# Performance work log

Hardware: AMD Instinct MI355X
Metric: run time of the kernel (lower is better)

The kernel has to match this reference:

```python
import jax, jax.numpy as jnp
import numpy as np

NUM_HEADS = 8
NUM_GROUPS = 8
EPS = 1e-5


def group_norm(x, weight, bias):
    B, C, T, H, W = x.shape
    xg = x.reshape(B, NUM_GROUPS, C // NUM_GROUPS, T, H, W)
    mean = xg.mean(axis=(2, 3, 4, 5), keepdims=True)
    var = xg.var(axis=(2, 3, 4, 5), keepdims=True)
    xg = (xg - mean) * jax.lax.rsqrt(var + EPS)
    x = xg.reshape(B, C, T, H, W)
    return x * weight[None, :, None, None, None] + bias[None, :, None, None, None]


def setup_inputs() -> dict:
    key = jax.random.key(0)
    ks = jax.random.split(key, 5)
    B, C, T, H, W = 4, 512, 16, 32, 32
    x = jax.random.normal(ks[0], (B, C, T, H, W), dtype=jnp.float32)
    gn_weight = jnp.ones((C,), dtype=jnp.float32)
    gn_bias = jnp.zeros((C,), dtype=jnp.float32)
    # 1x1x1 Conv3d weights collapse to dense (out, in) matrices
    qkv_w = jax.random.normal(ks[1], (3 * C, C), dtype=jnp.float32) * (1.0 / np.sqrt(C))
    qkv_b = jax.random.normal(ks[2], (3 * C,), dtype=jnp.float32) * 0.02
    out_w = jax.random.normal(ks[3], (C, C), dtype=jnp.float32) * (1.0 / np.sqrt(C))
    out_b = jax.random.normal(ks[4], (C,), dtype=jnp.float32) * 0.02
    return {"x": x, "gn_weight": gn_weight, "gn_bias": gn_bias,
            "qkv_w": qkv_w, "qkv_b": qkv_b, "out_w": out_w, "out_b": out_b}


def reference(x, gn_weight, gn_bias, qkv_w, qkv_b, out_w, out_b):
    B, C, T, H, W = x.shape
    nh = NUM_HEADS
    d = C // nh
    N = T * H * W

    h = group_norm(x, gn_weight, gn_bias)

    # 1x1x1 conv == pointwise channel matmul
    hf = h.reshape(B, C, N)                                  # [B, C, N]
    qkv = jnp.einsum('oc,bcn->bon', qkv_w, hf) + qkv_b[None, :, None]
    q, k, v = jnp.split(qkv, 3, axis=1)                      # each [B, C, N]
    q = q.reshape(B, nh, d, N)
    k = k.reshape(B, nh, d, N)
    v = v.reshape(B, nh, d, N)

    # NOTE: faithful to the torch code — contraction is over N (tokens),
    # giving a [B, nh, d, d] channel-attention matrix; softmax over last d.
    scale = d ** (-0.5)
    attn = jnp.einsum('bhdn,bhen->bhde', q, k) * scale       # [B, nh, d, d]
    attn = jax.nn.softmax(attn, axis=-1)
    out = jnp.einsum('bhde,bhen->bhdn', attn, v)             # [B, nh, d, N]

    out = out.reshape(B, C, N)
    out = jnp.einsum('oc,bcn->bon', out_w, out) + out_b[None, :, None]
    out = out.reshape(B, C, T, H, W)
    return x + out
```

## Files before the change

### kernel.cpp

```cpp
#include <hip/hip_runtime.h>
#include <hip/hip_fp16.h>


#define CCH 512
#define NTOK 16384
#define NHEAD 8

typedef _Float16 f16;
typedef _Float16 f16x8 __attribute__((ext_vector_type(8)));
typedef float f32x4 __attribute__((ext_vector_type(4)));

__device__ __forceinline__ void g2l16(const void* g, void* l) {
  __builtin_amdgcn_global_load_lds((const __attribute__((address_space(1))) void*)g,
                                   (__attribute__((address_space(3))) void*)l,
                                   16, 0, 0);
}

__global__ __launch_bounds__(256) void k_prep(const float* __restrict__ x,
                                              float* __restrict__ stats,
                                              const float* __restrict__ qkvw,
                                              f16* __restrict__ Wqkv16,
                                              const float* __restrict__ outw,
                                              f16* __restrict__ Ow16,
                                              f16* __restrict__ Wvt16) {
  __shared__ __align__(16) char smp[9216];
  int bid = blockIdx.x;
  int t = threadIdx.x;
  if (bid < 1024) {
    int chunk = bid & 31, bg = bid >> 5;
    const float4* p = (const float4*)(x + (size_t)bg * (64ull * NTOK)) + (size_t)chunk * 8192;
    float s = 0.f, q = 0.f;
    for (int i = t; i < 8192; i += 256) {
      float4 v = p[i];
      s += v.x + v.y + v.z + v.w;
      q += v.x * v.x + v.y * v.y + v.z * v.z + v.w * v.w;
    }
    for (int off = 32; off; off >>= 1) { s += __shfl_down(s, off); q += __shfl_down(q, off); }
    float* ls = (float*)smp; float* lq = ls + 4;
    int wid = t >> 6, lane = t & 63;
    if (lane == 0) { ls[wid] = s; lq[wid] = q; }
    __syncthreads();
    if (t == 0) {
      atomicAdd(&stats[bg * 2 + 0], ls[0] + ls[1] + ls[2] + ls[3]);
      atomicAdd(&stats[bg * 2 + 1], lq[0] + lq[1] + lq[2] + lq[3]);
    }
  } else if (bid < 2048) {
    bool isB = bid >= 1792;
    int i = (isB ? (bid - 1792) : (bid - 1024)) * 256 + t;
    const float* src = isB ? outw : qkvw;
    f16* dst = isB ? Ow16 : Wqkv16;
    float4 v = *(const float4*)&src[i * 4];
    f16 h[4] __attribute__((aligned(8)));
    h[0] = (f16)v.x; h[1] = (f16)v.y; h[2] = (f16)v.z; h[3] = (f16)v.w;
    *(uint2*)&dst[i * 4] = *(const uint2*)h;
  } else {
    int j = bid - 2048;
    int et = j >> 3, ct = j & 7;
    f16 (*tl)[72] = (f16(*)[72])smp;
    int r = t >> 2, cq = (t & 3) * 16;
    const float* src = &qkvw[(size_t)(1024 + et * 64 + r) * CCH + ct * 64 + cq];
#pragma unroll
    for (int k = 0; k < 4; ++k) {
      float4 v = *(const float4*)(src + k * 4);
      tl[r][cq + k * 4 + 0] = (f16)v.x; tl[r][cq + k * 4 + 1] = (f16)v.y;
      tl[r][cq + k * 4 + 2] = (f16)v.z; tl[r][cq + k * 4 + 3] = (f16)v.w;
    }
    __syncthreads();
    f16 hv[16] __attribute__((aligned(16)));
#pragma unroll
    for (int jj = 0; jj < 16; ++jj) hv[jj] = tl[cq + jj][r];
    f16* dst = &Wvt16[(size_t)(ct * 64 + r) * CCH + et * 64 + cq];
    *(uint4*)&dst[0] = ((const uint4*)hv)[0];
    *(uint4*)&dst[8] = ((const uint4*)hv)[1];
  }
}

__global__ __launch_bounds__(256) void k_gnorm(const float* __restrict__ x,
                                               const float* __restrict__ gw,
                                               const float* __restrict__ gb,
                                               const float* __restrict__ stats,
                                               f16* __restrict__ H, f16* __restrict__ Ht,
                                               float* __restrict__ svec) {
  int nc = blockIdx.x;
  int cg = blockIdx.y;
  int b = blockIdx.z;
  int t = threadIdx.x;
  __shared__ f16 T2[64][260];
  __shared__ float svp[4][64];
  float sum = stats[(b * 8 + cg) * 2], sq = stats[(b * 8 + cg) * 2 + 1];
  const float inv = 1.f / (64.f * (float)NTOK);
  float mean = sum * inv;
  float var = fmaxf(sq * inv - mean * mean, 0.f);
  float rsig = rsqrtf(var + 1e-5f);
  int c0 = cg * 64, n0 = nc * 256;
  int tq = t & 63, rr0 = t >> 6;
#pragma unroll
  for (int it = 0; it < 16; ++it) {
    int r = it * 4 + rr0;
    int c = c0 + r;
    float a = gw[c] * rsig;
    float bb = gb[c] - mean * a;
    size_t idx = ((size_t)(b * CCH + c)) * NTOK + n0 + tq * 4;
    float4 xv = *(const float4*)&x[idx];
    f16 hh[4] __attribute__((aligned(8)));
    hh[0] = (f16)(xv.x * a + bb);
    hh[1] = (f16)(xv.y * a + bb);
    hh[2] = (f16)(xv.z * a + bb);
    hh[3] = (f16)(xv.w * a + bb);
    *(uint2*)&H[idx] = *(const uint2*)hh;
    *(uint2*)&T2[r][tq * 4] = *(const uint2*)hh;
  }
  __syncthreads();
  {
    int c = t & 63, q = t >> 6;
    float acc = 0.f;
#pragma unroll
    for (int j = 0; j < 64; ++j) acc += (float)T2[c][q * 64 + j];
    svp[q][c] = acc;
  }
  __syncthreads();
  if (t < 64) {
    atomicAdd(&svec[b * CCH + c0 + t],
              svp[0][t] + svp[1][t] + svp[2][t] + svp[3][t]);
  }
  int s8 = t & 7, nl = t >> 3;
#pragma unroll
  for (int it = 0; it < 8; ++it) {
    int n = it * 32 + nl;
    f16 g[8] __attribute__((aligned(16)));
#pragma unroll
    for (int j = 0; j < 8; ++j) g[j] = T2[s8 * 8 + j][n];
    *(uint4*)&Ht[((size_t)b * NTOK + n0 + n) * CCH + c0 + s8 * 8] = *(const uint4*)g;
  }
}

#define SPLITS 16
__global__ __launch_bounds__(256, 2) void k_syrk(const f16* __restrict__ H,
                                                 float* __restrict__ G) {
  const int TI[10] = {0, 0, 0, 0, 1, 1, 1, 2, 2, 3};
  const int TJ[10] = {0, 1, 2, 3, 1, 2, 3, 2, 3, 3};
  int tile = blockIdx.x;
  int split = blockIdx.y;
  int b = blockIdx.z;
  int ii = TI[tile], jj = TJ[tile];
  int m0 = ii * 128, n0 = jj * 128;
  int t = threadIdx.x, lane = t & 63, wid = t >> 6;
  int wr = wid >> 1, wc = wid & 1;
  __shared__ __align__(16) f16 sA[128 * 64];
  __shared__ __align__(16) f16 sB[128 * 64];
  const f16* Hb = H + (size_t)b * CCH * NTOK;
  int k0 = split * (NTOK / SPLITS);
  f32x4 acc[4][4] = {};
  int ldsrow = wid * 8 + (lane >> 3);
  int slot = lane & 7;
  int lr = lane & 15, lk = lane >> 4;

  const int NS = (NTOK / SPLITS) / 64;
  for (int ks = 0; ks < NS; ++ks) {
    int kk0 = k0 + ks * 64;
    __syncthreads();
#pragma unroll
    for (int i = 0; i < 4; ++i) {
      int row = ldsrow + i * 32;
      int cA = ((slot ^ (row & 7)) * 8);
      g2l16(Hb + (size_t)(m0 + row) * NTOK + kk0 + cA, &sA[i * 2048 + wid * 512]);
      g2l16(Hb + (size_t)(n0 + row) * NTOK + kk0 + cA, &sB[i * 2048 + wid * 512]);
    }
    asm volatile("s_waitcnt vmcnt(0)" ::: "memory");
    __syncthreads();
#pragma unroll
    for (int kk = 0; kk < 2; ++kk) {
      f16x8 af[4], bf[4];
#pragma unroll
      for (int mi = 0; mi < 4; ++mi) {
        int row = wr * 64 + mi * 16 + lr;
        int ks8 = (kk * 4 + lk) ^ (row & 7);
        af[mi] = *(const f16x8*)&sA[row * 64 + ks8 * 8];
      }
#pragma unroll
      for (int ni = 0; ni < 4; ++ni) {
        int row = wc * 64 + ni * 16 + lr;
        int ks8 = (kk * 4 + lk) ^ (row & 7);
        bf[ni] = *(const f16x8*)&sB[row * 64 + ks8 * 8];
      }
#pragma unroll
      for (int mi = 0; mi < 4; ++mi)
#pragma unroll
        for (int ni = 0; ni < 4; ++ni)
          acc[mi][ni] = __builtin_amdgcn_mfma_f32_16x16x32_f16(af[mi], bf[ni], acc[mi][ni], 0, 0, 0);
    }
  }

  float* Gb = G + (size_t)b * CCH * CCH;
#pragma unroll
  for (int mi = 0; mi < 4; ++mi)
#pragma unroll
    for (int j = 0; j < 4; ++j) {
      int rr2 = m0 + wr * 64 + mi * 16 + lk * 4 + j;
#pragma unroll
      for (int ni = 0; ni < 4; ++ni) {
        int cc = n0 + wc * 64 + ni * 16 + lr;
        atomicAdd(&Gb[(size_t)rr2 * CCH + cc], acc[mi][ni][j]);
      }
    }
}

__global__ __launch_bounds__(256) void k_symm(float* __restrict__ G,
                                              f16* __restrict__ G16) {
  const int TI6[6] = {0, 0, 0, 1, 1, 2};
  const int TJ6[6] = {1, 2, 3, 2, 3, 3};
  int bx = blockIdx.x;
  int b = blockIdx.y;
  float* Gb = G + (size_t)b * CCH * CCH;
  f16* Gh = G16 + (size_t)b * CCH * CCH;
  __shared__ float s[64][65];
  int t = threadIdx.x;
  int r = t >> 2, cg = (t & 3) * 16;
  int ib, jb;
  bool mirror = bx < 24;
  if (mirror) {
    int t6 = bx >> 2, sub = bx & 3;
    ib = TI6[t6] * 2 + (sub >> 1); jb = TJ6[t6] * 2 + (sub & 1);
  } else {
    int idx = bx - 24; int dt = idx >> 2, sub = idx & 3;
    ib = dt * 2 + (sub >> 1); jb = dt * 2 + (sub & 1);
  }
  int grow = ib * 64 + r, gcol0 = jb * 64 + cg;
  const float* src = &Gb[(size_t)grow * CCH + gcol0];
  f16 hv[16] __attribute__((aligned(16)));
#pragma unroll
  for (int k = 0; k < 4; ++k) {
    float4 v = *(const float4*)(src + k * 4);
    if (mirror) {
      s[r][cg + k * 4 + 0] = v.x; s[r][cg + k * 4 + 1] = v.y;
      s[r][cg + k * 4 + 2] = v.z; s[r][cg + k * 4 + 3] = v.w;
    }
    hv[k * 4 + 0] = (f16)(v.x - ((grow == gcol0 + k * 4 + 0) ? 16384.f : 0.f));
    hv[k * 4 + 1] = (f16)(v.y - ((grow == gcol0 + k * 4 + 1) ? 16384.f : 0.f));
    hv[k * 4 + 2] = (f16)(v.z - ((grow == gcol0 + k * 4 + 2) ? 16384.f : 0.f));
    hv[k * 4 + 3] = (f16)(v.w - ((grow == gcol0 + k * 4 + 3) ? 16384.f : 0.f));
  }
  f16* d16 = &Gh[(size_t)grow * CCH + gcol0];
  *(uint4*)&d16[0] = ((const uint4*)hv)[0];
  *(uint4*)&d16[8] = ((const uint4*)hv)[1];
  if (mirror) {
    __syncthreads();
    float* dst = &Gb[(size_t)(jb * 64 + r) * CCH + ib * 64 + cg];
    f16 hw[16] __attribute__((aligned(16)));
#pragma unroll
    for (int k = 0; k < 4; ++k) {
      float4 v;
      v.x = s[cg + k * 4 + 0][r]; v.y = s[cg + k * 4 + 1][r];
      v.z = s[cg + k * 4 + 2][r]; v.w = s[cg + k * 4 + 3][r];
      *(float4*)(dst + k * 4) = v;
      hw[k * 4 + 0] = (f16)v.x; hw[k * 4 + 1] = (f16)v.y;
      hw[k * 4 + 2] = (f16)v.z; hw[k * 4 + 3] = (f16)v.w;
    }
    f16* m16 = &Gh[(size_t)(jb * 64 + r) * CCH + ib * 64 + cg];
    *(uint4*)&m16[0] = ((const uint4*)hw)[0];
    *(uint4*)&m16[8] = ((const uint4*)hw)[1];
  }
}

template <bool CORR>
__global__ __launch_bounds__(256, 2) void k_hgemm512(const f16* __restrict__ A16,
                                                     const f16* __restrict__ Bt16,
                                                     f16* __restrict__ Cv,
                                                     const float* __restrict__ corr) {
  int n0 = blockIdx.x * 128, m0 = blockIdx.y * 128, b = blockIdx.z;
  int t = threadIdx.x, lane = t & 63, wid = t >> 6;
  int wr = wid >> 1, wc = wid & 1;
  __shared__ __align__(16) f16 sA[128 * 64];
  __shared__ __align__(16) f16 sB[128 * 64];
  const f16* Bp = Bt16 + (size_t)b * CCH * CCH;
  f32x4 acc[4][4] = {};
  int ldsrow = wid * 8 + (lane >> 3);
  int slot = lane & 7;
  int lr = lane & 15, lk = lane >> 4;
  for (int ks = 0; ks < 8; ++ks) {
    int kk0 = ks * 64;
    __syncthreads();
#pragma unroll
    for (int i = 0; i < 4; ++i) {
      int row = ldsrow + i * 32;
      int cA = ((slot ^ (row & 7)) * 8);
      g2l16(A16 + (size_t)(m0 + row) * CCH + kk0 + cA, &sA[i * 2048 + wid * 512]);
      g2l16(Bp + (size_t)(n0 + row) * CCH + kk0 + cA, &sB[i * 2048 + wid * 512]);
    }
    asm volatile("s_waitcnt vmcnt(0)" ::: "memory");
    __syncthreads();
#pragma unroll
    for (int kk = 0; kk < 2; ++kk) {
      f16x8 af[4], bf[4];
#pragma unroll
      for (int mi = 0; mi < 4; ++mi) {
        int row = wr * 64 + mi * 16 + lr;
        int ks8 = (kk * 4 + lk) ^ (row & 7);
        af[mi] = *(const f16x8*)&sA[row * 64 + ks8 * 8];
      }
#pragma unroll
      for (int ni = 0; ni < 4; ++ni) {
        int row = wc * 64 + ni * 16 + lr;
        int ks8 = (kk * 4 + lk) ^ (row & 7);
        bf[ni] = *(const f16x8*)&sB[row * 64 + ks8 * 8];
      }
#pragma unroll
      for (int mi = 0; mi < 4; ++mi)
#pragma unroll
        for (int ni = 0; ni < 4; ++ni)
          acc[mi][ni] = __builtin_amdgcn_mfma_f32_16x16x32_f16(af[mi], bf[ni], acc[mi][ni], 0, 0, 0);
    }
  }
#pragma unroll
  for (int mi = 0; mi < 4; ++mi)
#pragma unroll
    for (int j = 0; j < 4; ++j) {
      int o = m0 + wr * 64 + mi * 16 + lk * 4 + j;
#pragma unroll
      for (int ni = 0; ni < 4; ++ni) {
        int n = n0 + wc * 64 + ni * 16 + lr;
        float v = acc[mi][ni][j];
        if constexpr (CORR) v += 16384.f * corr[(size_t)o * CCH + n];
        Cv[(size_t)b * CCH * CCH + (size_t)o * CCH + n] = (f16)v;
      }
    }
}

__global__ __launch_bounds__(256) void k_attn(const f16* __restrict__ T1h,
                                              const f16* __restrict__ Wqkv16,
                                              const f16* __restrict__ Wvt16,
                                              const float* __restrict__ qkvw,
                                              const float* __restrict__ qkvb,
                                              const float* __restrict__ svec,
                                              f16* __restrict__ Rt16,
                                              float* __restrict__ pbv) {
  int h = blockIdx.x, b = blockIdx.y;
  int h64 = h * 64;
  int t = threadIdx.x, lane = t & 63, wid = t >> 6;
  int lr = lane & 15, lk = lane >> 4;
  __shared__ float ss[512];
  __shared__ float suq[64], suk[64], sbq[64], sbk[64], sbv[64];
  __shared__ float Lsm[64][68];
  __shared__ f16 Psm[64][72];

  for (int i = t; i < 512; i += 256) ss[i] = svec[b * CCH + i];
  if (t < 64) {
    sbq[t] = qkvb[h64 + t];
    sbk[t] = qkvb[512 + h64 + t];
    sbv[t] = qkvb[1024 + h64 + t];
  }
  __syncthreads();
  if (t < 128) {
    int o = t & 63; bool isk = t >= 64;
    const float* wr_ = qkvw + (size_t)((isk ? 512 : 0) + h64 + o) * CCH;
    float a = 0.f;
#pragma unroll
    for (int i = 0; i < 128; ++i) {
      float4 w = *(const float4*)&wr_[i * 4];
      a += w.x * ss[i * 4] + w.y * ss[i * 4 + 1] + w.z * ss[i * 4 + 2] + w.w * ss[i * 4 + 3];
    }
    (isk ? suk : suq)[o] = a;
  }
  int wr = wid >> 1, wc = wid & 1;
  f32x4 lacc[2][2] = {};
  const f16* Ab = T1h + (size_t)b * CCH * CCH;
  const f16* Bb = Wqkv16 + (size_t)(512 + h64) * CCH;
  for (int ks = 0; ks < 16; ++ks) {
    int kq = ks * 32 + lk * 8;
    f16x8 af[2], bf[2];
#pragma unroll
    for (int mi = 0; mi < 2; ++mi)
      af[mi] = *(const f16x8*)&Ab[(size_t)(h64 + wr * 32 + mi * 16 + lr) * CCH + kq];
#pragma unroll
    for (int ni = 0; ni < 2; ++ni)
      bf[ni] = *(const f16x8*)&Bb[(size_t)(wc * 32 + ni * 16 + lr) * CCH + kq];
#pragma unroll
    for (int mi = 0; mi < 2; ++mi)
#pragma unroll
      for (int ni = 0; ni < 2; ++ni)
        lacc[mi][ni] = __builtin_amdgcn_mfma_f32_16x16x32_f16(af[mi], bf[ni], lacc[mi][ni], 0, 0, 0);
  }
  __syncthreads();
#pragma unroll
  for (int mi = 0; mi < 2; ++mi)
#pragma unroll
    for (int ni = 0; ni < 2; ++ni)
#pragma unroll
      for (int j = 0; j < 4; ++j) {
        int d = wr * 32 + mi * 16 + lk * 4 + j;
        int e = wc * 32 + ni * 16 + lr;
        Lsm[d][e] = (lacc[mi][ni][j] + suq[d] * sbk[e] + sbq[d] * suk[e]
                     + 16384.f * sbq[d] * sbk[e]) * 0.125f;
      }
  __syncthreads();
  if (t < 64) {
    float m = -1e30f;
#pragma unroll
    for (int e = 0; e < 64; ++e) m = fmaxf(m, Lsm[t][e]);
    float p[64];
    float sum = 0.f;
#pragma unroll
    for (int e = 0; e < 64; ++e) { p[e] = expf(Lsm[t][e] - m); sum += p[e]; }
    float r = 1.f / sum, pb = 0.f;
#pragma unroll
    for (int e = 0; e < 64; ++e) {
      float pv = p[e] * r;
      Psm[t][e] = (f16)pv;
      pb += pv * sbv[e];
    }
    pbv[b * CCH + h64 + t] = pb;
  }
  __syncthreads();
  f32x4 acc[4][8] = {};
  int c0w = wid * 128;
#pragma unroll
  for (int kk = 0; kk < 2; ++kk) {
    int e0 = kk * 32 + lk * 8;
    f16x8 pa[4], wb[8];
#pragma unroll
    for (int mi = 0; mi < 4; ++mi)
      pa[mi] = *(const f16x8*)&Psm[mi * 16 + lr][e0];
#pragma unroll
    for (int ni = 0; ni < 8; ++ni)
      wb[ni] = *(const f16x8*)&Wvt16[(size_t)(c0w + ni * 16 + lr) * CCH + h64 + e0];
#pragma unroll
    for (int mi = 0; mi < 4; ++mi)
#pragma unroll
      for (int ni = 0; ni < 8; ++ni)
        acc[mi][ni] = __builtin_amdgcn_mfma_f32_16x16x32_f16(pa[mi], wb[ni], acc[mi][ni], 0, 0, 0);
  }
#pragma unroll
  for (int mi = 0; mi < 4; ++mi)
#pragma unroll
    for (int ni = 0; ni < 8; ++ni) {
      int d0 = mi * 16 + lk * 4;
      int c = c0w + ni * 16 + lr;
      f16 hv[4] __attribute__((aligned(8)));
#pragma unroll
      for (int j = 0; j < 4; ++j) hv[j] = (f16)acc[mi][ni][j];
      *(uint2*)&Rt16[((size_t)b * CCH + c) * CCH + h64 + d0] = *(const uint2*)hv;
    }
}

__global__ __launch_bounds__(256) void k_cvec(const float* __restrict__ outw,
                                              const float* __restrict__ outb,
                                              const float* __restrict__ pbv,
                                              float* __restrict__ cvec) {
  int o = blockIdx.x * 64 + (threadIdx.x >> 2);
  int l = threadIdx.x & 3;
  int b = blockIdx.y;
  __shared__ float sp[512];
  for (int i = threadIdx.x; i < 512; i += 256) sp[i] = pbv[b * CCH + i];
  __syncthreads();
  const float* wr_ = outw + (size_t)o * CCH + l * 128;
  const float* spp = sp + l * 128;
  float a = 0.f;
#pragma unroll
  for (int i = 0; i < 32; ++i) {
    float4 w = *(const float4*)&wr_[i * 4];
    a += w.x * spp[i * 4] + w.y * spp[i * 4 + 1] + w.z * spp[i * 4 + 2] + w.w * spp[i * 4 + 3];
  }
  a += __shfl_down(a, 2);
  a += __shfl_down(a, 1);
  if (l == 0) cvec[b * CCH + o] = a + outb[o];
}

__global__ __launch_bounds__(256, 2) void k_out(const f16* __restrict__ M16,
                                                const f16* __restrict__ Ht,
                                                const float* __restrict__ x,
                                                const float* __restrict__ cvec,
                                                float* __restrict__ out) {
  int nt = blockIdx.x;
  int mt = blockIdx.y;
  int b = blockIdx.z;
  int m0 = mt * 128, n0 = nt * 128;
  int t = threadIdx.x, lane = t & 63, wid = t >> 6;
  int wr = wid >> 1, wc = wid & 1;
  __shared__ __align__(16) f16 sA[128 * 64];
  __shared__ __align__(16) f16 sB[128 * 64];
  const f16* A = M16 + (size_t)b * CCH * CCH;
  const f16* Bp = Ht + (size_t)b * NTOK * CCH;
  f32x4 acc[4][4] = {};
  int ldsrow = wid * 8 + (lane >> 3);
  int slot = lane & 7;
  int lr = lane & 15, lk = lane >> 4;
  for (int ks = 0; ks < 8; ++ks) {
    int kk0 = ks * 64;
    __syncthreads();
#pragma unroll
    for (int i = 0; i < 4; ++i) {
      int row = ldsrow + i * 32;
      int cA = ((slot ^ (row & 7)) * 8);
      g2l16(A + (size_t)(m0 + row) * CCH + kk0 + cA, &sA[i * 2048 + wid * 512]);
      g2l16(Bp + (size_t)(n0 + row) * CCH + kk0 + cA, &sB[i * 2048 + wid * 512]);
    }
    asm volatile("s_waitcnt vmcnt(0)" ::: "memory");
    __syncthreads();
#pragma unroll
    for (int kk = 0; kk < 2; ++kk) {
      f16x8 af[4], bf[4];
#pragma unroll
      for (int mi = 0; mi < 4; ++mi) {
        int row = wr * 64 + mi * 16 + lr;
        int ks8 = (kk * 4 + lk) ^ (row & 7);
        af[mi] = *(const f16x8*)&sA[row * 64 + ks8 * 8];
      }
#pragma unroll
      for (int ni = 0; ni < 4; ++ni) {
        int row = wc * 64 + ni * 16 + lr;
        int ks8 = (kk * 4 + lk) ^ (row & 7);
        bf[ni] = *(const f16x8*)&sB[row * 64 + ks8 * 8];
      }
#pragma unroll
      for (int mi = 0; mi < 4; ++mi)
#pragma unroll
        for (int ni = 0; ni < 4; ++ni)
          acc[mi][ni] = __builtin_amdgcn_mfma_f32_16x16x32_f16(bf[ni], af[mi], acc[mi][ni], 0, 0, 0);
    }
  }

  const float* xb = x + ((size_t)b * CCH) * NTOK;
  float* ob = out + ((size_t)b * CCH) * NTOK;
#pragma unroll
  for (int mi = 0; mi < 4; ++mi) {
    int o = m0 + wr * 64 + mi * 16 + lr;
    float cv = cvec[b * CCH + o];
    size_t rowoff = (size_t)o * NTOK;
#pragma unroll
    for (int ni = 0; ni < 4; ++ni) {
      int n = n0 + wc * 64 + ni * 16 + lk * 4;
      float4 xv = *(const float4*)&xb[rowoff + n];
      float4 ov;
      ov.x = xv.x + acc[mi][ni][0] + cv;
      ov.y = xv.y + acc[mi][ni][1] + cv;
      ov.z = xv.z + acc[mi][ni][2] + cv;
      ov.w = xv.w + acc[mi][ni][3] + cv;
      *(float4*)&ob[rowoff + n] = ov;
    }
  }
}

extern "C" void kernel_launch(void* const* d_in, const int* in_sizes, int n_in,
                              void* d_out, int out_size, void* d_ws, size_t ws_size,
                              hipStream_t stream) {
  const float* x    = (const float*)d_in[0];
  const float* gw   = (const float*)d_in[1];
  const float* gb   = (const float*)d_in[2];
  const float* qkvw = (const float*)d_in[3];
  const float* qkvb = (const float*)d_in[4];
  const float* outw = (const float*)d_in[5];
  const float* outb = (const float*)d_in[6];
  int B = in_sizes[0] / (CCH * NTOK);

  char* ws = (char*)d_ws;
  size_t off = 0;
  f16* H      = (f16*)(ws + off);   off += (size_t)B * CCH * NTOK * 2;
  f16* Ht     = (f16*)(ws + off);   off += (size_t)B * NTOK * CCH * 2;
  float* G    = (float*)(ws + off); off += (size_t)B * CCH * CCH * 4;
  f16* G16    = (f16*)(ws + off);   off += (size_t)B * CCH * CCH * 2;
  f16* T1h    = (f16*)(ws + off);   off += (size_t)B * CCH * CCH * 2;
  f16* Rt16   = (f16*)(ws + off);   off += (size_t)B * CCH * CCH * 2;
  f16* M16    = (f16*)(ws + off);   off += (size_t)B * CCH * CCH * 2;
  f16* Wqkv16 = (f16*)(ws + off);   off += (size_t)3 * CCH * CCH * 2;
  f16* Ow16   = (f16*)(ws + off);   off += (size_t)CCH * CCH * 2;
  f16* Wvt16  = (f16*)(ws + off);   off += (size_t)CCH * CCH * 2;
  float* pbv  = (float*)(ws + off); off += (size_t)B * CCH * 4;
  float* cvec = (float*)(ws + off); off += (size_t)B * CCH * 4;
  float* stats = (float*)(ws + off); off += (size_t)B * 8 * 2 * 4;
  float* svec  = (float*)(ws + off); off += (size_t)B * CCH * 4;
  size_t zbytes = (size_t)(B * 8 * 2 + B * CCH) * 4;

  hipMemsetAsync(G, 0, (size_t)B * CCH * CCH * 4, stream);
  hipMemsetAsync(stats, 0, zbytes, stream);

  k_prep<<<dim3(2112), 256, 0, stream>>>(x, stats, qkvw, Wqkv16, outw, Ow16, Wvt16);
  k_gnorm<<<dim3(64, 8, B), 256, 0, stream>>>(x, gw, gb, stats, H, Ht, svec);
  k_syrk<<<dim3(10, SPLITS, B), 256, 0, stream>>>(H, G);
  k_symm<<<dim3(40, B), 256, 0, stream>>>(G, G16);
  k_hgemm512<true><<<dim3(4, 4, B), 256, 0, stream>>>(Wqkv16, G16, T1h, qkvw);
  k_attn<<<dim3(NHEAD, B), 256, 0, stream>>>(T1h, Wqkv16, Wvt16, qkvw, qkvb, svec,
                                             Rt16, pbv);
  k_hgemm512<false><<<dim3(4, 4, B), 256, 0, stream>>>(Ow16, Rt16, M16, nullptr);
  k_cvec<<<dim3(8, B), 256, 0, stream>>>(outw, outb, pbv, cvec);
  k_out<<<dim3(128, 4, B), 256, 0, stream>>>(M16, Ht, x, cvec, (float*)d_out);
}
```

Baseline: 299.7 us.

## Fold group-norm affine algebraically into Gram and output GEMMs, removing a pass over x

Instead of a stats pass followed by a separate normalize pass, the prep kernel now reads x once and does three things: it accumulates group stats, converts raw x to f16 (plus a transposed copy), and computes per-channel sums. The per-channel norm scale and shift are applied afterwards. They enter the Gram matrix as a rank-one correction in the symmetrize kernel, a scale factor in the second GEMM epilogue, and a bias adjustment via a new small kernel. This removes one full read of x and the dependency between the two passes, and the symmetrize kernel no longer writes mirrored fp32 data. The risk is precision: the Gram is now computed on unnormalized f16 x, so the mean-related cancellation in the correction terms could lose accuracy.

```diff
diff --git a/kernel.cpp b/kernel.cpp
--- a/kernel.cpp
+++ b/kernel.cpp
@@ -16,37 +16,73 @@
                                    16, 0, 0);
 }
 
-__global__ __launch_bounds__(256) void k_prep(const float* __restrict__ x,
-                                              float* __restrict__ stats,
-                                              const float* __restrict__ qkvw,
-                                              f16* __restrict__ Wqkv16,
-                                              const float* __restrict__ outw,
-                                              f16* __restrict__ Ow16,
-                                              f16* __restrict__ Wvt16) {
-  __shared__ __align__(16) char smp[9216];
+__global__ __launch_bounds__(256) void k_prep2(const float* __restrict__ x,
+                                               float* __restrict__ stats,
+                                               float* __restrict__ sx,
+                                               f16* __restrict__ x16,
+                                               f16* __restrict__ xt16,
+                                               const float* __restrict__ qkvw,
+                                               f16* __restrict__ Wqkv16,
+                                               const float* __restrict__ outw,
+                                               f16* __restrict__ Ow16,
+                                               f16* __restrict__ Wvt16) {
+  __shared__ __align__(16) char smp[34816];
   int bid = blockIdx.x;
   int t = threadIdx.x;
-  if (bid < 1024) {
-    int chunk = bid & 31, bg = bid >> 5;
-    const float4* p = (const float4*)(x + (size_t)bg * (64ull * NTOK)) + (size_t)chunk * 8192;
+  if (bid < 2048) {
+    f16 (*T2)[260] = (f16(*)[260])smp;
+    float (*svp)[64] = (float(*)[64])(smp + 33280);
+    float* lsq = (float*)(smp + 34304);
+    int nc = bid & 63, cg = (bid >> 6) & 7, b = bid >> 9;
+    int c0 = cg * 64, n0 = nc * 256;
+    int tq = t & 63, rr0 = t >> 6;
     float s = 0.f, q = 0.f;
-    for (int i = t; i < 8192; i += 256) {
-      float4 v = p[i];
-      s += v.x + v.y + v.z + v.w;
-      q += v.x * v.x + v.y * v.y + v.z * v.z + v.w * v.w;
+#pragma unroll
+    for (int it = 0; it < 16; ++it) {
+      int r = it * 4 + rr0;
+      int c = c0 + r;
+      size_t idx = ((size_t)(b * CCH + c)) * NTOK + n0 + tq * 4;
+      float4 xv = *(const float4*)&x[idx];
+      s += xv.x + xv.y + xv.z + xv.w;
+      q += xv.x * xv.x + xv.y * xv.y + xv.z * xv.z + xv.w * xv.w;
+      f16 hh[4] __attribute__((aligned(8)));
+      hh[0] = (f16)xv.x; hh[1] = (f16)xv.y; hh[2] = (f16)xv.z; hh[3] = (f16)xv.w;
+      *(uint2*)&x16[idx] = *(const uint2*)hh;
+      *(uint2*)&T2[r][tq * 4] = *(const uint2*)hh;
     }
     for (int off = 32; off; off >>= 1) { s += __shfl_down(s, off); q += __shfl_down(q, off); }
-    float* ls = (float*)smp; float* lq = ls + 4;
     int wid = t >> 6, lane = t & 63;
-    if (lane == 0) { ls[wid] = s; lq[wid] = q; }
+    if (lane == 0) { lsq[wid] = s; lsq[4 + wid] = q; }
     __syncthreads();
     if (t == 0) {
-      atomicAdd(&stats[bg * 2 + 0], ls[0] + ls[1] + ls[2] + ls[3]);
-      atomicAdd(&stats[bg * 2 + 1], lq[0] + lq[1] + lq[2] + lq[3]);
-    }
-  } else if (bid < 2048) {
-    bool isB = bid >= 1792;
-    int i = (isB ? (bid - 1792) : (bid - 1024)) * 256 + t;
+      atomicAdd(&stats[(b * 8 + cg) * 2 + 0], lsq[0] + lsq[1] + lsq[2] + lsq[3]);
+      atomicAdd(&stats[(b * 8 + cg) * 2 + 1], lsq[4] + lsq[5] + lsq[6] + lsq[7]);
+    }
+    {
+      int c = t & 63, qd = t >> 6;
+      float acc = 0.f;
+#pragma unroll
+      for (int j = 0; j < 64; ++j) acc += (float)T2[c][qd * 64 + j];
+      svp[qd][c] = acc;
+    }
+    __syncthreads();
+    if (t < 64) {
+      atomicAdd(&sx[b * CCH + c0 + t],
+                svp[0][t] + svp[1][t] + svp[2][t] + svp[3][t]);
+    }
+    int s8 = t & 7, nl = t >> 3;
+#pragma unroll
+    for (int it = 0; it < 8; ++it) {
+      int n = it * 32 + nl;
+      f16 g[8] __attribute__((aligned(16)));
+#pragma unroll
+      for (int j = 0; j < 8; ++j) g[j] = T2[s8 * 8 + j][n];
+      *(uint4*)&xt16[((size_t)b * NTOK + n0 + n) * CCH + c0 + s8 * 8] = *(const uint4*)g;
+    }
+  } else if (bid < 3072) {
+    int bid2 = bid - 2048;
+    bool isB = bid2 >= 768;
+    int i = (isB ? (bid2 - 768) : bid2) * 256 + t;
     const float* src = isB ? outw : qkvw;
     f16* dst = isB ? Ow16 : Wqkv16;
     float4 v = *(const float4*)&src[i * 4];
@@ -54,7 +90,7 @@
     h[0] = (f16)v.x; h[1] = (f16)v.y; h[2] = (f16)v.z; h[3] = (f16)v.w;
     *(uint2*)&dst[i * 4] = *(const uint2*)h;
   } else {
-    int j = bid - 2048;
+    int j = bid - 3072;
     int et = j >> 3, ct = j & 7;
     f16 (*tl)[72] = (f16(*)[72])smp;
     int r = t >> 2, cq = (t & 3) * 16;
@@ -75,63 +111,56 @@
   }
 }
 
-__global__ __launch_bounds__(256) void k_gnorm(const float* __restrict__ x,
-                                               const float* __restrict__ gw,
-                                               const float* __restrict__ gb,
-                                               const float* __restrict__ stats,
-                                               f16* __restrict__ H, f16* __restrict__ Ht,
-                                               float* __restrict__ svec) {
-  int nc = blockIdx.x;
-  int cg = blockIdx.y;
-  int b = blockIdx.z;
+__global__ __launch_bounds__(256) void k_ab(const float* __restrict__ stats,
+                                            const float* __restrict__ gw,
+                                            const float* __restrict__ gb,
+                                            const float* __restrict__ sx,
+                                            const float* __restrict__ qkvw,
+                                            float* __restrict__ avec,
+                                            float* __restrict__ bvec,
+                                            float* __restrict__ asxv,
+                                            float* __restrict__ svecH,
+                                            float* __restrict__ yvec) {
+  int ob = blockIdx.x, b = blockIdx.y;
   int t = threadIdx.x;
-  __shared__ f16 T2[64][260];
-  __shared__ float svp[4][64];
-  float sum = stats[(b * 8 + cg) * 2], sq = stats[(b * 8 + cg) * 2 + 1];
-  const float inv = 1.f / (64.f * (float)NTOK);
-  float mean = sum * inv;
-  float var = fmaxf(sq * inv - mean * mean, 0.f);
-  float rsig = rsqrtf(var + 1e-5f);
-  int c0 = cg * 64, n0 = nc * 256;
-  int tq = t & 63, rr0 = t >> 6;
-#pragma unroll
-  for (int it = 0; it < 16; ++it) {
-    int r = it * 4 + rr0;
-    int c = c0 + r;
-    float a = gw[c] * rsig;
-    float bb = gb[c] - mean * a;
-    size_t idx = ((size_t)(b * CCH + c)) * NTOK + n0 + tq * 4;
-    float4 xv = *(const float4*)&x[idx];
-    f16 hh[4] __attribute__((aligned(8)));
-    hh[0] = (f16)(xv.x * a + bb);
-    hh[1] = (f16)(xv.y * a + bb);
-    hh[2] = (f16)(xv.z * a + bb);
-    hh[3] = (f16)(xv.w * a + bb);
-    *(uint2*)&H[idx] = *(const uint2*)hh;
-    *(uint2*)&T2[r][tq * 4] = *(const uint2*)hh;
+  __shared__ float smean[8], srsig[8], sb[512];
+  if (t < 8) {
+    const float inv = 1.f / (64.f * (float)NTOK);
+    float sum = stats[(b * 8 + t) * 2], sq = stats[(b * 8 + t) * 2 + 1];
+    float mean = sum * inv;
+    float var = fmaxf(sq * inv - mean * mean, 0.f);
+    smean[t] = mean; srsig[t] = rsqrtf(var + 1e-5f);
   }
   __syncthreads();
-  {
-    int c = t & 63, q = t >> 6;
-    float acc = 0.f;
-#pragma unroll
-    for (int j = 0; j < 64; ++j) acc += (float)T2[c][q * 64 + j];
-    svp[q][c] = acc;
+  for (int c = t; c < 512; c += 256) {
+    int g = c >> 6;
+    float a = gw[c] * srsig[g];
+    sb[c] = gb[c] - smean[g] * a;
   }
   __syncthreads();
   if (t < 64) {
-    atomicAdd(&svec[b * CCH + c0 + t],
-              svp[0][t] + svp[1][t] + svp[2][t] + svp[3][t]);
-  }
-  int s8 = t & 7, nl = t >> 3;
-#pragma unroll
-  for (int it = 0; it < 8; ++it) {
-    int n = it * 32 + nl;
-    f16 g[8] __attribute__((aligned(16)));
-#pragma unroll
-    for (int j = 0; j < 8; ++j) g[j] = T2[s8 * 8 + j][n];
-    *(uint4*)&Ht[((size_t)b * NTOK + n0 + n) * CCH + c0 + s8 * 8] = *(const uint4*)g;
-  }
+    int c = ob * 64 + t; int g = c >> 6;
+    float a = gw[c] * srsig[g];
+    float bb = sb[c];
+    float sxc = sx[b * CCH + c];
+    avec[b * CCH + c] = a;
+    bvec[b * CCH + c] = bb;
+    asxv[b * CCH + c] = a * sxc;
+    svecH[b * CCH + c] = a * sxc + (float)NTOK * bb;
+  }
+  int e = ob * 64 + (t >> 2);
+  int l = t & 3;
+  const float* wr_ = qkvw + (size_t)(1024 + e) * CCH + l * 128;
+  const float* sbb = sb + l * 128;
+  float acc = 0.f;
+#pragma unroll
+  for (int i = 0; i < 32; ++i) {
+    float4 w = *(const float4*)&wr_[i * 4];
+    acc += w.x * sbb[i * 4] + w.y * sbb[i * 4 + 1] + w.z * sbb[i * 4 + 2] + w.w * sbb[i * 4 + 3];
+  }
+  acc += __shfl_down(acc, 2);
+  acc += __shfl_down(acc, 1);
+  if (l == 0) yvec[b * CCH + e] = acc;
 }
 
 #define SPLITS 16
@@ -205,14 +234,20 @@
     }
 }
 
-__global__ __launch_bounds__(256) void k_symm(float* __restrict__ G,
-                                              f16* __restrict__ G16) {
+__global__ __launch_bounds__(256) void k_symm2(const float* __restrict__ X,
+                                               const float* __restrict__ avec,
+                                               const float* __restrict__ bvec,
+                                               const float* __restrict__ asxv,
+                                               f16* __restrict__ G16) {
   const int TI6[6] = {0, 0, 0, 1, 1, 2};
   const int TJ6[6] = {1, 2, 3, 2, 3, 3};
   int bx = blockIdx.x;
   int b = blockIdx.y;
-  float* Gb = G + (size_t)b * CCH * CCH;
+  const float* Xb = X + (size_t)b * CCH * CCH;
   f16* Gh = G16 + (size_t)b * CCH * CCH;
+  const float* av = avec + b * CCH;
+  const float* bv = bvec + b * CCH;
+  const float* asx = asxv + b * CCH;
   __shared__ float s[64][65];
   int t = threadIdx.x;
   int r = t >> 2, cg = (t & 3) * 16;
@@ -226,36 +261,31 @@
     ib = dt * 2 + (sub >> 1); jb = dt * 2 + (sub & 1);
   }
   int grow = ib * 64 + r, gcol0 = jb * 64 + cg;
-  const float* src = &Gb[(size_t)grow * CCH + gcol0];
+  float ar = av[grow], br = bv[grow], asxr = asx[grow];
+  const float* src = &Xb[(size_t)grow * CCH + gcol0];
   f16 hv[16] __attribute__((aligned(16)));
 #pragma unroll
   for (int k = 0; k < 4; ++k) {
-    float4 v = *(const float4*)(src + k * 4);
-    if (mirror) {
-      s[r][cg + k * 4 + 0] = v.x; s[r][cg + k * 4 + 1] = v.y;
-      s[r][cg + k * 4 + 2] = v.z; s[r][cg + k * 4 + 3] = v.w;
-    }
-    hv[k * 4 + 0] = (f16)(v.x - ((grow == gcol0 + k * 4 + 0) ? 16384.f : 0.f));
-    hv[k * 4 + 1] = (f16)(v.y - ((grow == gcol0 + k * 4 + 1) ? 16384.f : 0.f));
-    hv[k * 4 + 2] = (f16)(v.z - ((grow == gcol0 + k * 4 + 2) ? 16384.f : 0.f));
-    hv[k * 4 + 3] = (f16)(v.w - ((grow == gcol0 + k * 4 + 3) ? 16384.f : 0.f));
+    float4 xv = *(const float4*)(src + k * 4);
+    float vv[4] = {xv.x, xv.y, xv.z, xv.w};
+#pragma unroll
+    for (int i = 0; i < 4; ++i) {
+      int cc = gcol0 + k * 4 + i;
+      float v = ar * av[cc] * vv[i] + asxr * bv[cc] + br * asx[cc]
+                + (float)NTOK * br * bv[cc];
+      if (grow == cc) v -= 16384.f;
+      hv[k * 4 + i] = (f16)v;
+      if (mirror) s[r][cg + k * 4 + i] = v;
+    }
   }
   f16* d16 = &Gh[(size_t)grow * CCH + gcol0];
   *(uint4*)&d16[0] = ((const uint4*)hv)[0];
   *(uint4*)&d16[8] = ((const uint4*)hv)[1];
   if (mirror) {
     __syncthreads();
-    float* dst = &Gb[(size_t)(jb * 64 + r) * CCH + ib * 64 + cg];
     f16 hw[16] __attribute__((aligned(16)));
 #pragma unroll
-    for (int k = 0; k < 4; ++k) {
-      float4 v;
-      v.x = s[cg + k * 4 + 0][r]; v.y = s[cg + k * 4 + 1][r];
-      v.z = s[cg + k * 4 + 2][r]; v.w = s[cg + k * 4 + 3][r];
-      *(float4*)(dst + k * 4) = v;
-      hw[k * 4 + 0] = (f16)v.x; hw[k * 4 + 1] = (f16)v.y;
-      hw[k * 4 + 2] = (f16)v.z; hw[k * 4 + 3] = (f16)v.w;
-    }
+    for (int k = 0; k < 16; ++k) hw[k] = (f16)s[cg + k][r];
     f16* m16 = &Gh[(size_t)(jb * 64 + r) * CCH + ib * 64 + cg];
     *(uint4*)&m16[0] = ((const uint4*)hw)[0];
     *(uint4*)&m16[8] = ((const uint4*)hw)[1];
@@ -266,7 +296,8 @@
 __global__ __launch_bounds__(256, 2) void k_hgemm512(const f16* __restrict__ A16,
                                                      const f16* __restrict__ Bt16,
                                                      f16* __restrict__ Cv,
-                                                     const float* __restrict__ corr) {
+                                                     const float* __restrict__ corr,
+                                                     const float* __restrict__ ascale) {
   int n0 = blockIdx.x * 128, m0 = blockIdx.y * 128, b = blockIdx.z;
   int t = threadIdx.x, lane = t & 63, wid = t >> 6;
   int wr = wid >> 1, wc = wid & 1;
@@ -321,6 +352,7 @@
         int n = n0 + wc * 64 + ni * 16 + lr;
         float v = acc[mi][ni][j];
         if constexpr (CORR) v += 16384.f * corr[(size_t)o * CCH + n];
+        else                v *= ascale[(size_t)b * CCH + n];
         Cv[(size_t)b * CCH * CCH + (size_t)o * CCH + n] = (f16)v;
       }
     }
@@ -332,6 +364,7 @@
                                               const float* __restrict__ qkvw,
                                               const float* __restrict__ qkvb,
                                               const float* __restrict__ svec,
+                                              const float* __restrict__ yvec,
                                               f16* __restrict__ Rt16,
                                               float* __restrict__ pbv) {
   int h = blockIdx.x, b = blockIdx.y;
@@ -347,7 +380,7 @@
   if (t < 64) {
     sbq[t] = qkvb[h64 + t];
     sbk[t] = qkvb[512 + h64 + t];
-    sbv[t] = qkvb[1024 + h64 + t];
+    sbv[t] = qkvb[1024 + h64 + t] + yvec[b * CCH + h64 + t];
   }
   __syncthreads();
   if (t < 128) {
@@ -554,9 +587,9 @@
 
   char* ws = (char*)d_ws;
   size_t off = 0;
-  f16* H      = (f16*)(ws + off);   off += (size_t)B * CCH * NTOK * 2;
-  f16* Ht     = (f16*)(ws + off);   off += (size_t)B * NTOK * CCH * 2;
-  float* G    = (float*)(ws + off); off += (size_t)B * CCH * CCH * 4;
+  f16* x16    = (f16*)(ws + off);   off += (size_t)B * CCH * NTOK * 2;
+  f16* xt16   = (f16*)(ws + off);   off += (size_t)B * NTOK * CCH * 2;
+  float* X    = (float*)(ws + off); off += (size_t)B * CCH * CCH * 4;
   f16* G16    = (f16*)(ws + off);   off += (size_t)B * CCH * CCH * 2;
   f16* T1h    = (f16*)(ws + off);   off += (size_t)B * CCH * CCH * 2;
   f16* Rt16   = (f16*)(ws + off);   off += (size_t)B * CCH * CCH * 2;
@@ -564,23 +597,30 @@
   f16* Wqkv16 = (f16*)(ws + off);   off += (size_t)3 * CCH * CCH * 2;
   f16* Ow16   = (f16*)(ws + off);   off += (size_t)CCH * CCH * 2;
   f16* Wvt16  = (f16*)(ws + off);   off += (size_t)CCH * CCH * 2;
+  float* avec = (float*)(ws + off); off += (size_t)B * CCH * 4;
+  float* bvec = (float*)(ws + off); off += (size_t)B * CCH * 4;
+  float* asxv = (float*)(ws + off); off += (size_t)B * CCH * 4;
+  float* svecH= (float*)(ws + off); off += (size_t)B * CCH * 4;
+  float* yvec = (float*)(ws + off); off += (size_t)B * CCH * 4;
   float* pbv  = (float*)(ws + off); off += (size_t)B * CCH * 4;
   float* cvec = (float*)(ws + off); off += (size_t)B * CCH * 4;
   float* stats = (float*)(ws + off); off += (size_t)B * 8 * 2 * 4;
-  float* svec  = (float*)(ws + off); off += (size_t)B * CCH * 4;
+  float* sx    = (float*)(ws + off); off += (size_t)B * CCH * 4;
   size_t zbytes = (size_t)(B * 8 * 2 + B * CCH) * 4;
 
-  hipMemsetAsync(G, 0, (size_t)B * CCH * CCH * 4, stream);
+  hipMemsetAsync(X, 0, (size_t)B * CCH * CCH * 4, stream);
   hipMemsetAsync(stats, 0, zbytes, stream);
 
-  k_prep<<<dim3(2112), 256, 0, stream>>>(x, stats, qkvw, Wqkv16, outw, Ow16, Wvt16);
-  k_gnorm<<<dim3(64, 8, B), 256, 0, stream>>>(x, gw, gb, stats, H, Ht, svec);
-  k_syrk<<<dim3(10, SPLITS, B), 256, 0, stream>>>(H, G);
-  k_symm<<<dim3(40, B), 256, 0, stream>>>(G, G16);
-  k_hgemm512<true><<<dim3(4, 4, B), 256, 0, stream>>>(Wqkv16, G16, T1h, qkvw);
-  k_attn<<<dim3(NHEAD, B), 256, 0, stream>>>(T1h, Wqkv16, Wvt16, qkvw, qkvb, svec,
-                                             Rt16, pbv);
-  k_hgemm512<false><<<dim3(4, 4, B), 256, 0, stream>>>(Ow16, Rt16, M16, nullptr);
+  k_prep2<<<dim3(3136), 256, 0, stream>>>(x, stats, sx, x16, xt16,
+                                          qkvw, Wqkv16, outw, Ow16, Wvt16);
+  k_ab<<<dim3(8, B), 256, 0, stream>>>(stats, gw, gb, sx, qkvw,
+                                       avec, bvec, asxv, svecH, yvec);
+  k_syrk<<<dim3(10, SPLITS, B), 256, 0, stream>>>(x16, X);
+  k_symm2<<<dim3(40, B), 256, 0, stream>>>(X, avec, bvec, asxv, G16);
+  k_hgemm512<true><<<dim3(4, 4, B), 256, 0, stream>>>(Wqkv16, G16, T1h, qkvw, nullptr);
+  k_attn<<<dim3(NHEAD, B), 256, 0, stream>>>(T1h, Wqkv16, Wvt16, qkvw, qkvb,
+                                             svecH, yvec, Rt16, pbv);
+  k_hgemm512<false><<<dim3(4, 4, B), 256, 0, stream>>>(Ow16, Rt16, M16, nullptr, avec);
   k_cvec<<<dim3(8, B), 256, 0, stream>>>(outw, outb, pbv, cvec);
-  k_out<<<dim3(128, 4, B), 256, 0, stream>>>(M16, Ht, x, cvec, (float*)d_out);
-}
+  k_out<<<dim3(128, 4, B), 256, 0, stream>>>(M16, xt16, x, cvec, (float*)d_out);
+}
```

New measurement: 277.2 us. 1.08x faster.
